# Kernel optimization log

Measured on AMD Instinct MI355X. Metric: run time of the kernel, lower is better.

The kernel has to match this reference:

```python
import jax, jax.numpy as jnp
import numpy as np

DIM = 256
NUM_HEADS = 4
HEAD_DIM = DIM // NUM_HEADS
SCALE = HEAD_DIM ** -0.5


def setup_inputs() -> dict:
    key = jax.random.key(0)
    ks = jax.random.split(key, 6)
    B, S = 4, 4096
    x = jax.random.normal(ks[0], (B, S, DIM), dtype=jnp.float32)
    # nn.Linear weights are [out, in]; we store them that way and apply x @ W.T
    wq = jax.random.normal(ks[1], (DIM, DIM), dtype=jnp.float32) * (DIM ** -0.5)
    wk = jax.random.normal(ks[2], (DIM, DIM), dtype=jnp.float32) * (DIM ** -0.5)
    wv = jax.random.normal(ks[3], (DIM, DIM), dtype=jnp.float32) * (DIM ** -0.5)
    wo = jax.random.normal(ks[4], (DIM, DIM), dtype=jnp.float32) * (DIM ** -0.5)
    bo = jax.random.normal(ks[5], (DIM,), dtype=jnp.float32) * 0.02
    return {"x": x, "wq": wq, "wk": wk, "wv": wv, "wo": wo, "bo": bo}


def reference(x, wq, wk, wv, wo, bo):
    B, S, D = x.shape
    H, Hd = NUM_HEADS, HEAD_DIM
    # project and split heads: [B, H, S, Hd]
    q = (x @ wq.T).reshape(B, S, H, Hd).transpose(0, 2, 1, 3)
    k = (x @ wk.T).reshape(B, S, H, Hd).transpose(0, 2, 1, 3)
    v = (x @ wv.T).reshape(B, S, H, Hd).transpose(0, 2, 1, 3)
    attn = jnp.einsum('bhqd,bhkd->bhqk', q, k) * SCALE
    attn = jax.nn.softmax(attn, axis=-1)  # dropout is identity in eval mode
    out = jnp.einsum('bhqk,bhkd->bhqd', attn, v)
    out = out.transpose(0, 2, 1, 3).reshape(B, S, D)
    return out @ wo.T + bo
```

## Files before the change

### kernel.cpp

```cpp
#include <hip/hip_runtime.h>
#include <hip/hip_bf16.h>
#include <stdint.h>

#define DIM    256
#define NH     4
#define HD     64
#define BATCH  4
#define SEQ    4096
#define NTOK   (BATCH*SEQ)

typedef __bf16    bf16_t;
typedef _Float16  f16_t;
typedef _Float16  f16x8  __attribute__((ext_vector_type(8)));
typedef _Float16  f16x4  __attribute__((ext_vector_type(4)));
typedef float     f32x4  __attribute__((ext_vector_type(4)));
typedef unsigned short u16x8 __attribute__((ext_vector_type(8)));

#define MFMA_F16    __builtin_amdgcn_mfma_f32_16x16x32_f16
#define MFMA_F16_16 __builtin_amdgcn_mfma_f32_16x16x16f16

#define QSCALE 0.18033688011112042f

#define WS_XA    ((size_t)0)
#define WS_Q     ((size_t)4194304)
#define WS_K     ((size_t)8388608)
#define WS_VT    ((size_t)12582912)
#define WS_W     ((size_t)16777216)
#define WS_BO    ((size_t)17039360)
#define WS_OATT  WS_XA

#define LSTRIDE 72
#define KBUF    4608

__device__ __forceinline__ size_t tiled_idx(int row, int k) {
  return ((size_t)(row >> 4) * 32 + (k >> 3)) * 128 + (row & 15) * 8 + (k & 7);
}

__device__ __forceinline__ int detect_mode(const uint32_t* wq_u32) {
  uint32_t word = wq_u32[(threadIdx.x & 63) * 431 + 17];
  uint32_t b = (word >> 8) & 0x7fu;
  unsigned long long m = __ballot(b >= 0x38u && b <= 0x3fu);
  return (__popcll(m) >= 32) ? 0 : 1;
}

__device__ __forceinline__ f16x8 cvt_chunk(const void* src, size_t elem, int mode) {
  f16x8 r;
  if (mode) {
    const float* s = (const float*)src + elem;
    #pragma unroll
    for (int j = 0; j < 8; ++j) r[j] = (f16_t)s[j];
  } else {
    u16x8 v = *(const u16x8*)((const unsigned short*)src + elem);
    #pragma unroll
    for (int j = 0; j < 8; ++j) r[j] = (f16_t)__uint_as_float(((unsigned)v[j]) << 16);
  }
  return r;
}

__global__ __launch_bounds__(256) void cvt_all_kernel(
    const void* __restrict__ x,
    const void* __restrict__ wq, const void* __restrict__ wk,
    const void* __restrict__ wv, const void* __restrict__ wo,
    const void* __restrict__ bo,
    f16_t* __restrict__ xA, f16_t* __restrict__ wT,
    float* __restrict__ bof) {
  __shared__ int s_mode;
  if (threadIdx.x < 64) {
    int m = detect_mode((const uint32_t*)wq);
    if (threadIdx.x == 0) s_mode = m;
  }
  __syncthreads();
  const int mode = s_mode;
  const int bid = blockIdx.x;

  if (bid < 2048) {
    int idx = bid * 256 + (int)threadIdx.x;
    int tok = idx >> 5, kc = idx & 31;
    f16x8 r = cvt_chunk(x, (size_t)tok * DIM + kc * 8, mode);
    *(f16x8*)(xA + tiled_idx(tok, kc * 8)) = r;
  } else if (bid < 2176) {
    int idx = (bid - 2048) * 256 + (int)threadIdx.x;
    int which = idx >> 13, local = idx & 8191;
    const void* src = (which == 0) ? wq : (which == 1) ? wk : (which == 2) ? wv : wo;
    int n = local >> 5, kc = local & 31;
    f16x8 r = cvt_chunk(src, (size_t)n * DIM + kc * 8, mode);
    *(f16x8*)(wT + (size_t)which * 65536 + tiled_idx(n, kc * 8)) = r;
  } else {
    int i = threadIdx.x;
    bof[i] = mode ? ((const float*)bo)[i] : (float)((const bf16_t*)bo)[i];
  }
}

__global__ __launch_bounds__(256) void proj_fused_kernel(
    const f16_t* __restrict__ xA, const f16_t* __restrict__ wT,
    f16_t* __restrict__ q, f16_t* __restrict__ kk, f16_t* __restrict__ vt) {
  const int z    = blockIdx.z;
  const f16_t* w = wT + (size_t)z * 65536;
  const int lane = threadIdx.x & 63;
  const int wvi  = threadIdx.x >> 6;
  const int c    = lane & 15;
  const int g    = lane >> 4;

  if (z < 2) {
    const float scale = (z == 0) ? QSCALE : 1.0f;
    f16_t* out = (z == 0) ? q : kk;
    const int m0 = blockIdx.x * 64 + wvi * 16;
    const int n0 = blockIdx.y * 64;
    const f16_t* abase = xA + (size_t)(m0 >> 4) * 4096 + c * 8;
    const f16_t* bbase = w + (size_t)(n0 >> 4) * 4096 + c * 8;
    f32x4 acc[4] = {};
    #pragma unroll
    for (int ks = 0; ks < 8; ++ks) {
      const int kc = (ks * 4 + g) * 128;
      f16x8 a = *(const f16x8*)(abase + kc);
      #pragma unroll
      for (int nt = 0; nt < 4; ++nt) {
        f16x8 b = *(const f16x8*)(bbase + (size_t)nt * 4096 + kc);
        acc[nt] = MFMA_F16(a, b, acc[nt], 0, 0, 0);
      }
    }
    #pragma unroll
    for (int nt = 0; nt < 4; ++nt) {
      const int n = n0 + nt * 16 + c;
      const int h = n >> 6, d = n & 63;
      #pragma unroll
      for (int r = 0; r < 4; ++r) {
        const int tok = m0 + g * 4 + r;
        const int b = tok >> 12, s = tok & 4095;
        out[(size_t)((b * NH + h) * SEQ + s) * HD + d] = (f16_t)(acc[nt][r] * scale);
      }
    }
  } else {
    const int m0 = blockIdx.y * 64 + wvi * 16;
    const int n0 = blockIdx.x * 64;
    const f16_t* abase = w + (size_t)(m0 >> 4) * 4096 + c * 8;
    const f16_t* bbase = xA + (size_t)(n0 >> 4) * 4096 + c * 8;
    f32x4 acc[4] = {};
    #pragma unroll
    for (int ks = 0; ks < 8; ++ks) {
      const int kc = (ks * 4 + g) * 128;
      f16x8 a = *(const f16x8*)(abase + kc);
      #pragma unroll
      for (int nt = 0; nt < 4; ++nt) {
        f16x8 b = *(const f16x8*)(bbase + (size_t)nt * 4096 + kc);
        acc[nt] = MFMA_F16(a, b, acc[nt], 0, 0, 0);
      }
    }
    #pragma unroll
    for (int nt = 0; nt < 4; ++nt) {
      const int tok = n0 + nt * 16 + c;
      const int b = tok >> 12, s = tok & 4095;
      #pragma unroll
      for (int r = 0; r < 4; ++r) {
        const int vd = m0 + g * 4 + r;
        const int h = vd >> 6, d = vd & 63;
        vt[(size_t)((b * NH + h) * HD + d) * SEQ + s] = (f16_t)acc[nt][r];
      }
    }
  }
}

__global__ __launch_bounds__(256, 4) void attn_kernel(
    const f16_t* __restrict__ q, const f16_t* __restrict__ k,
    const f16_t* __restrict__ vt, f16_t* __restrict__ o) {
  __shared__ __align__(16) f16_t smem[18432];

  const int tid  = threadIdx.x;
  const int lane = tid & 63;
  const int w    = tid >> 6;
  const int wq_  = w & 1;
  const int wk_  = w >> 1;
  const int c    = lane & 15;
  const int g    = lane >> 4;
  const int bh   = blockIdx.x;
  const int q0   = blockIdx.y * 64;

  const f16_t* qb = q + (size_t)(bh * SEQ + q0 + wq_ * 32 + c) * HD;
  f16x8 qf[2][2];
  #pragma unroll
  for (int qt = 0; qt < 2; ++qt) {
    qf[qt][0] = *(const f16x8*)(qb + (size_t)(qt * 16) * HD + g * 8);
    qf[qt][1] = *(const f16x8*)(qb + (size_t)(qt * 16) * HD + 32 + g * 8);
  }

  const int r0 = tid >> 3, ch = tid & 7;
  const f16_t* kg0 = k  + (size_t)bh * SEQ * HD + (size_t)r0 * HD + ch * 8;
  const f16_t* kg1 = kg0 + (size_t)32 * HD;
  const f16_t* vg0 = vt + (size_t)bh * HD * SEQ + (size_t)r0 * SEQ + ch * 8;
  const f16_t* vg1 = vg0 + (size_t)32 * SEQ;
  const int kst  = r0 * LSTRIDE + ch * 8;
  const int kst2 = (r0 + 32) * LSTRIDE + ch * 8;

  f32x4 oacc[8] = {};
  float lpart[2] = {};

  {
    uint4 ka  = *(const uint4*)(kg0);
    uint4 kb2 = *(const uint4*)(kg1);
    uint4 va  = *(const uint4*)(vg0);
    uint4 vb2 = *(const uint4*)(vg1);
    *(uint4*)(smem + kst)         = ka;
    *(uint4*)(smem + kst2)        = kb2;
    *(uint4*)(smem + KBUF + kst)  = va;
    *(uint4*)(smem + KBUF + kst2) = vb2;
  }
  __syncthreads();

  const int kAbase = (wk_ * 32 + c) * LSTRIDE + g * 8;
  const int vAbase = wk_ * 32 + g * 4;

  for (int kt = 0; kt < SEQ / 64; ++kt) {
    const int cur = (kt & 1) * (2 * KBUF);
    const int nxt = ((kt & 1) ^ 1) * (2 * KBUF);
    uint4 ka4, kb4, va4, vb4;
    const bool more = (kt < SEQ / 64 - 1);
    if (more) {
      const size_t ko = (size_t)(kt + 1) * 64 * HD;
      const size_t vo = (size_t)(kt + 1) * 64;
      ka4 = *(const uint4*)(kg0 + ko);
      kb4 = *(const uint4*)(kg1 + ko);
      va4 = *(const uint4*)(vg0 + vo);
      vb4 = *(const uint4*)(vg1 + vo);
    }

    f16x8 kfa[2][2];
    #pragma unroll
    for (int kts = 0; kts < 2; ++kts) {
      const f16_t* kl = smem + cur + kAbase + kts * 16 * LSTRIDE;
      kfa[kts][0] = *(const f16x8*)(kl);
      kfa[kts][1] = *(const f16x8*)(kl + 32);
    }
    f16x4 vfr[4][2];
    #pragma unroll
    for (int dt = 0; dt < 4; ++dt)
      #pragma unroll
      for (int kts = 0; kts < 2; ++kts)
        vfr[dt][kts] = *(const f16x4*)(smem + cur + KBUF +
                                       (dt * 16 + c) * LSTRIDE + vAbase + kts * 16);

    f16x4 pk[2][2];
    #pragma unroll
    for (int kts = 0; kts < 2; ++kts) {
      #pragma unroll
      for (int qt = 0; qt < 2; ++qt) {
        f32x4 st = {};
        st = MFMA_F16(kfa[kts][0], qf[qt][0], st, 0, 0, 0);
        st = MFMA_F16(kfa[kts][1], qf[qt][1], st, 0, 0, 0);
        float p0 = __builtin_amdgcn_exp2f(st[0]);
        float p1 = __builtin_amdgcn_exp2f(st[1]);
        float p2 = __builtin_amdgcn_exp2f(st[2]);
        float p3 = __builtin_amdgcn_exp2f(st[3]);
        lpart[qt] += (p0 + p1) + (p2 + p3);
        f16x4 pv = { (f16_t)p0, (f16_t)p1, (f16_t)p2, (f16_t)p3 };
        pk[kts][qt] = pv;
      }
    }
    #pragma unroll
    for (int dt = 0; dt < 4; ++dt)
      #pragma unroll
      for (int qt = 0; qt < 2; ++qt) {
        f32x4 acc = oacc[dt * 2 + qt];
        acc = MFMA_F16_16(vfr[dt][0], pk[0][qt], acc, 0, 0, 0);
        acc = MFMA_F16_16(vfr[dt][1], pk[1][qt], acc, 0, 0, 0);
        oacc[dt * 2 + qt] = acc;
      }

    if (more) {
      *(uint4*)(smem + nxt + kst)         = ka4;
      *(uint4*)(smem + nxt + kst2)        = kb4;
      *(uint4*)(smem + nxt + KBUF + kst)  = va4;
      *(uint4*)(smem + nxt + KBUF + kst2) = vb4;
    }
    __syncthreads();
  }

  float* red   = (float*)smem;
  float* lred_ = (float*)(smem + 16384);

  float lw[2];
  #pragma unroll
  for (int qt = 0; qt < 2; ++qt) {
    float lv = lpart[qt];
    lv += __shfl_xor(lv, 16);
    lv += __shfl_xor(lv, 32);
    lw[qt] = lv;
  }
  if (lane < 16) {
    #pragma unroll
    for (int qt = 0; qt < 2; ++qt) lred_[w * 32 + qt * 16 + lane] = lw[qt];
  }
  if (wk_ == 1) {
    float* dst = red + wq_ * 2048;
    #pragma unroll
    for (int i = 0; i < 8; ++i) *(f32x4*)(dst + i * 256 + lane * 4) = oacc[i];
  }
  __syncthreads();
  if (wk_ == 0) {
    const float* s = red + wq_ * 2048;
    #pragma unroll
    for (int i = 0; i < 8; ++i) oacc[i] += *(const f32x4*)(s + i * 256 + lane * 4);
    float inv[2];
    #pragma unroll
    for (int qt = 0; qt < 2; ++qt)
      inv[qt] = 1.0f / (lred_[w * 32 + qt * 16 + c] + lred_[(w + 2) * 32 + qt * 16 + c]);

    const int b = bh >> 2, h = bh & 3;
    #pragma unroll
    for (int dt = 0; dt < 4; ++dt) {
      #pragma unroll
      for (int qt = 0; qt < 2; ++qt) {
        f32x4 v = oacc[dt * 2 + qt];
        f16x4 ov = { (f16_t)(v[0] * inv[qt]), (f16_t)(v[1] * inv[qt]),
                     (f16_t)(v[2] * inv[qt]), (f16_t)(v[3] * inv[qt]) };
        const int mt = b * 256 + blockIdx.y * 4 + wq_ * 2 + qt;
        const int kc = h * 8 + dt * 2 + (g >> 1);
        *(f16x4*)(o + ((size_t)mt * 32 + kc) * 128 + c * 8 + (g & 1) * 4) = ov;
      }
    }
  }
}

__global__ __launch_bounds__(256) void out_proj_kernel(
    const f16_t* __restrict__ aA, const f16_t* __restrict__ wT,
    const float* __restrict__ bo, void* __restrict__ outv,
    const void* __restrict__ wq_raw) {
  __shared__ int s_mode;
  if (threadIdx.x < 64) {
    int m = detect_mode((const uint32_t*)wq_raw);
    if (threadIdx.x == 0) s_mode = m;
  }
  __syncthreads();
  const int mode = s_mode;

  const int lane = threadIdx.x & 63;
  const int wv   = threadIdx.x >> 6;
  const int c    = lane & 15;
  const int g    = lane >> 4;
  const int m0   = blockIdx.x * 64 + wv * 16;
  const int n0   = blockIdx.y * 64;

  const f16_t* abase = aA + (size_t)(m0 >> 4) * 4096 + c * 8;
  const f16_t* bbase = wT + (size_t)(n0 >> 4) * 4096 + c * 8;
  f32x4 acc[4] = {};

  #pragma unroll
  for (int ks = 0; ks < 8; ++ks) {
    const int kc = (ks * 4 + g) * 128;
    f16x8 a = *(const f16x8*)(abase + kc);
    #pragma unroll
    for (int nt = 0; nt < 4; ++nt) {
      f16x8 b = *(const f16x8*)(bbase + (size_t)nt * 4096 + kc);
      acc[nt] = MFMA_F16(a, b, acc[nt], 0, 0, 0);
    }
  }

  #pragma unroll
  for (int nt = 0; nt < 4; ++nt) {
    const int n = n0 + nt * 16 + c;
    const float bias = bo[n];
    #pragma unroll
    for (int r = 0; r < 4; ++r) {
      const int tok = m0 + g * 4 + r;
      const float val = acc[nt][r] + bias;
      const size_t idx = (size_t)tok * DIM + n;
      if (mode) ((float*)outv)[idx] = val;
      else      ((bf16_t*)outv)[idx] = (bf16_t)val;
    }
  }
}

extern "C" void kernel_launch(void* const* d_in, const int* in_sizes, int n_in,
                              void* d_out, int out_size, void* d_ws, size_t ws_size,
                              hipStream_t stream) {
  (void)in_sizes; (void)n_in; (void)out_size; (void)ws_size;
  const void* x  = d_in[0];
  const void* wq = d_in[1];
  const void* wk = d_in[2];
  const void* wv = d_in[3];
  const void* wo = d_in[4];
  const void* bo = d_in[5];

  f16_t* ws    = (f16_t*)d_ws;
  f16_t* xA    = ws + WS_XA;
  f16_t* q     = ws + WS_Q;
  f16_t* kk    = ws + WS_K;
  f16_t* vt    = ws + WS_VT;
  f16_t* wT    = ws + WS_W;
  f16_t* woT   = ws + WS_W + 196608;
  float* bof   = (float*)(ws + WS_BO);
  f16_t* oattA = ws + WS_OATT;

  cvt_all_kernel   <<<dim3(2177),      256, 0, stream>>>(x, wq, wk, wv, wo, bo,
                                                         xA, wT, bof);
  proj_fused_kernel<<<dim3(256, 4, 3), 256, 0, stream>>>(xA, wT, q, kk, vt);
  attn_kernel      <<<dim3(16, 64),    256, 0, stream>>>(q, kk, vt, oattA);
  out_proj_kernel  <<<dim3(256, 4),    256, 0, stream>>>(oattA, woT, bof, d_out, wq);
}
```

Baseline: 201.3 us.

## Rewrite attention with 32x32 MFMA, 128-query tiles and pre-swizzled K/V layouts

The attention kernel moves from 16x16 MFMA tiles to 32x32x16 MFMA, and each block now covers 128 queries instead of 64, halving the grid. The projection kernel writes K and V in a 64-row tile image with an XOR-swizzled chunk order, so the attention kernel can copy each tile to LDS contiguously and read it without bank conflicts. P fragments are rearranged in registers with permlane32 swaps. The aim is fewer MFMA issues, less LDS padding and cheaper loads, at the cost of more registers per thread (launch bounds drop to 2 blocks per CU) and a more intricate layout contract between kernels. Softmax still omits max subtraction, as before.

```diff
diff --git a/kernel.cpp b/kernel.cpp
--- a/kernel.cpp
+++ b/kernel.cpp
@@ -14,10 +14,14 @@
 typedef _Float16  f16x8  __attribute__((ext_vector_type(8)));
 typedef _Float16  f16x4  __attribute__((ext_vector_type(4)));
 typedef float     f32x4  __attribute__((ext_vector_type(4)));
+typedef float     f32x16 __attribute__((ext_vector_type(16)));
 typedef unsigned short u16x8 __attribute__((ext_vector_type(8)));
+typedef unsigned int   u32;
+typedef u32 u32x2 __attribute__((ext_vector_type(2)));
+typedef u32 u32x4 __attribute__((ext_vector_type(4)));
 
 #define MFMA_F16    __builtin_amdgcn_mfma_f32_16x16x32_f16
-#define MFMA_F16_16 __builtin_amdgcn_mfma_f32_16x16x16f16
+#define MFMA32_F16  __builtin_amdgcn_mfma_f32_32x32x16_f16
 
 #define QSCALE 0.18033688011112042f
 
@@ -29,9 +33,6 @@
 #define WS_BO    ((size_t)17039360)
 #define WS_OATT  WS_XA
 
-#define LSTRIDE 72
-#define KBUF    4608
-
 __device__ __forceinline__ size_t tiled_idx(int row, int k) {
   return ((size_t)(row >> 4) * 32 + (k >> 3)) * 128 + (row & 15) * 8 + (k & 7);
 }
@@ -55,6 +56,24 @@
     for (int j = 0; j < 8; ++j) r[j] = (f16_t)__uint_as_float(((unsigned)v[j]) << 16);
   }
   return r;
+}
+
+__device__ __forceinline__ u32 pkh(float a, float b) {
+  auto h = __builtin_amdgcn_cvt_pkrtz(a, b);
+  return __builtin_bit_cast(u32, h);
+}
+
+__device__ __forceinline__ void swap32(u32& x, u32& y) {
+#if __has_builtin(__builtin_amdgcn_permlane32_swap)
+  u32x2 r = __builtin_amdgcn_permlane32_swap(x, y, false, false);
+  x = r[0]; y = r[1];
+#else
+  u32 xp = __shfl_xor((int)x, 32), yp = __shfl_xor((int)y, 32);
+  const bool h = (threadIdx.x & 32) != 0;
+  u32 nx = h ? yp : x;
+  u32 ny = h ? y  : xp;
+  x = nx; y = ny;
+#endif
 }
 
 __global__ __launch_bounds__(256) void cvt_all_kernel(
@@ -103,7 +122,6 @@
 
   if (z < 2) {
     const float scale = (z == 0) ? QSCALE : 1.0f;
-    f16_t* out = (z == 0) ? q : kk;
     const int m0 = blockIdx.x * 64 + wvi * 16;
     const int n0 = blockIdx.y * 64;
     const f16_t* abase = xA + (size_t)(m0 >> 4) * 4096 + c * 8;
@@ -119,15 +137,32 @@
         acc[nt] = MFMA_F16(a, b, acc[nt], 0, 0, 0);
       }
     }
-    #pragma unroll
-    for (int nt = 0; nt < 4; ++nt) {
-      const int n = n0 + nt * 16 + c;
-      const int h = n >> 6, d = n & 63;
-      #pragma unroll
-      for (int r = 0; r < 4; ++r) {
-        const int tok = m0 + g * 4 + r;
-        const int b = tok >> 12, s = tok & 4095;
-        out[(size_t)((b * NH + h) * SEQ + s) * HD + d] = (f16_t)(acc[nt][r] * scale);
+    if (z == 0) {
+      #pragma unroll
+      for (int nt = 0; nt < 4; ++nt) {
+        const int n = n0 + nt * 16 + c;
+        const int h = n >> 6, d = n & 63;
+        #pragma unroll
+        for (int r = 0; r < 4; ++r) {
+          const int tok = m0 + g * 4 + r;
+          const int b = tok >> 12, s = tok & 4095;
+          q[(size_t)((b * NH + h) * SEQ + s) * HD + d] = (f16_t)(acc[nt][r] * scale);
+        }
+      }
+    } else {
+      #pragma unroll
+      for (int nt = 0; nt < 4; ++nt) {
+        const int n = n0 + nt * 16 + c;
+        const int h = n >> 6, d = n & 63;
+        #pragma unroll
+        for (int r = 0; r < 4; ++r) {
+          const int tok = m0 + g * 4 + r;
+          const int b = tok >> 12, s = tok & 4095;
+          const int kt = s >> 6, row = s & 63;
+          const int ch = (d >> 3) ^ (row & 7);
+          kk[(size_t)(b * NH + h) * (SEQ * HD) + kt * 4096 + row * 64 + ch * 8 + (d & 7)]
+              = (f16_t)acc[nt][r];
+        }
       }
     }
   } else {
@@ -150,173 +185,176 @@
     for (int nt = 0; nt < 4; ++nt) {
       const int tok = n0 + nt * 16 + c;
       const int b = tok >> 12, s = tok & 4095;
+      const int kt = s >> 6, ko = s & 63;
       #pragma unroll
       for (int r = 0; r < 4; ++r) {
         const int vd = m0 + g * 4 + r;
         const int h = vd >> 6, d = vd & 63;
-        vt[(size_t)((b * NH + h) * HD + d) * SEQ + s] = (f16_t)acc[nt][r];
-      }
-    }
-  }
-}
-
-__global__ __launch_bounds__(256, 4) void attn_kernel(
-    const f16_t* __restrict__ q, const f16_t* __restrict__ k,
-    const f16_t* __restrict__ vt, f16_t* __restrict__ o) {
-  __shared__ __align__(16) f16_t smem[18432];
-
-  const int tid  = threadIdx.x;
-  const int lane = tid & 63;
-  const int w    = tid >> 6;
-  const int wq_  = w & 1;
-  const int wk_  = w >> 1;
-  const int c    = lane & 15;
-  const int g    = lane >> 4;
-  const int bh   = blockIdx.x;
-  const int q0   = blockIdx.y * 64;
-
-  const f16_t* qb = q + (size_t)(bh * SEQ + q0 + wq_ * 32 + c) * HD;
-  f16x8 qf[2][2];
+        const int ch = (ko >> 3) ^ (d & 7);
+        vt[(size_t)(b * NH + h) * (SEQ * HD) + kt * 4096 + d * 64 + ch * 8 + (ko & 7)]
+            = (f16_t)acc[nt][r];
+      }
+    }
+  }
+}
+
+__global__ __launch_bounds__(256, 2) void attn_kernel(
+    const f16_t* __restrict__ q, const f16_t* __restrict__ kimg,
+    const f16_t* __restrict__ vimg, f16_t* __restrict__ o) {
+  __shared__ __align__(16) f16_t smem[16896];
+
+  const int tid = threadIdx.x;
+  const int l   = tid & 63;
+  const int w   = tid >> 6;
+  const int wq_ = w & 1;
+  const int wk_ = w >> 1;
+  const int ql  = l & 31;
+  const int hi  = l >> 5;
+  const int bh  = blockIdx.x;
+  const int q0  = blockIdx.y * 128;
+
+  const f16_t* qb = q + ((size_t)bh * SEQ + q0 + wq_ * 64 + ql) * HD + hi * 8;
+  f16x8 qf[2][4];
+  #pragma unroll
+  for (int qt = 0; qt < 2; ++qt)
+    #pragma unroll
+    for (int s = 0; s < 4; ++s)
+      qf[qt][s] = *(const f16x8*)(qb + (size_t)qt * 32 * HD + s * 16);
+
+  const bool isv = tid >= 128;
+  const f16_t* gsrc = (isv ? vimg : kimg) + (size_t)bh * (SEQ * HD) + (tid & 127) * 32;
+  f16_t* ldst = smem + (isv ? 4096 : 0) + (tid & 127) * 32;
+
+  const int qx  = ql & 7;
+  const int krow = wk_ * 32 + ql;
+  int koff[4], voff[2][2];
+  #pragma unroll
+  for (int s = 0; s < 4; ++s)
+    koff[s] = krow * 64 + (((s * 2 + hi) ^ qx) * 8);
+  #pragma unroll
+  for (int dt = 0; dt < 2; ++dt) {
+    const int drow = dt * 32 + ql;
+    #pragma unroll
+    for (int kb = 0; kb < 2; ++kb)
+      voff[dt][kb] = 4096 + drow * 64 + (((wk_ * 4 + kb * 2 + hi) ^ qx) * 8);
+  }
+
+  f32x16 acc[2][2] = {};
+  float lsum[2] = {0.f, 0.f};
+
+  {
+    const uint4* gg = (const uint4*)gsrc;
+    uint4* dd = (uint4*)ldst;
+    dd[0] = gg[0]; dd[1] = gg[1]; dd[2] = gg[2]; dd[3] = gg[3];
+  }
+  __syncthreads();
+
+  for (int kt = 0; kt < SEQ / 64; ++kt) {
+    const int bufo = (kt & 1) * 8192;
+    const bool more = kt < SEQ / 64 - 1;
+    uint4 s0, s1, s2, s3;
+    if (more) {
+      const uint4* gg = (const uint4*)(gsrc + (size_t)(kt + 1) * 4096);
+      s0 = gg[0]; s1 = gg[1]; s2 = gg[2]; s3 = gg[3];
+    }
+
+    f16x8 kf[4], vf[2][2];
+    #pragma unroll
+    for (int s = 0; s < 4; ++s)
+      kf[s] = *(const f16x8*)(smem + bufo + koff[s]);
+    #pragma unroll
+    for (int dt = 0; dt < 2; ++dt)
+      #pragma unroll
+      for (int kb = 0; kb < 2; ++kb)
+        vf[dt][kb] = *(const f16x8*)(smem + bufo + voff[dt][kb]);
+
+    f16x8 pf[2][2];
+    #pragma unroll
+    for (int qt = 0; qt < 2; ++qt) {
+      f32x16 st = {};
+      #pragma unroll
+      for (int s = 0; s < 4; ++s) st = MFMA32_F16(kf[s], qf[qt][s], st, 0, 0, 0);
+      float p[16];
+      #pragma unroll
+      for (int r = 0; r < 16; ++r) p[r] = __builtin_amdgcn_exp2f(st[r]);
+      float ls = 0.f;
+      #pragma unroll
+      for (int r = 0; r < 16; r += 4) ls += (p[r] + p[r + 1]) + (p[r + 2] + p[r + 3]);
+      lsum[qt] += ls;
+      #pragma unroll
+      for (int kb = 0; kb < 2; ++kb) {
+        u32 d0 = pkh(p[kb * 8 + 0], p[kb * 8 + 1]);
+        u32 d1 = pkh(p[kb * 8 + 2], p[kb * 8 + 3]);
+        u32 d2 = pkh(p[kb * 8 + 4], p[kb * 8 + 5]);
+        u32 d3 = pkh(p[kb * 8 + 6], p[kb * 8 + 7]);
+        swap32(d0, d2);
+        swap32(d1, d3);
+        u32x4 fd; fd[0] = d0; fd[1] = d1; fd[2] = d2; fd[3] = d3;
+        pf[qt][kb] = __builtin_bit_cast(f16x8, fd);
+      }
+    }
+
+    #pragma unroll
+    for (int dt = 0; dt < 2; ++dt)
+      #pragma unroll
+      for (int qt = 0; qt < 2; ++qt) {
+        f32x16 a = acc[dt][qt];
+        a = MFMA32_F16(vf[dt][0], pf[qt][0], a, 0, 0, 0);
+        a = MFMA32_F16(vf[dt][1], pf[qt][1], a, 0, 0, 0);
+        acc[dt][qt] = a;
+      }
+
+    if (more) {
+      uint4* dd = (uint4*)(ldst + (bufo ^ 8192));
+      dd[0] = s0; dd[1] = s1; dd[2] = s2; dd[3] = s3;
+    }
+    __syncthreads();
+  }
+
+  float* lred = (float*)(smem + 16384);
   #pragma unroll
   for (int qt = 0; qt < 2; ++qt) {
-    qf[qt][0] = *(const f16x8*)(qb + (size_t)(qt * 16) * HD + g * 8);
-    qf[qt][1] = *(const f16x8*)(qb + (size_t)(qt * 16) * HD + 32 + g * 8);
-  }
-
-  const int r0 = tid >> 3, ch = tid & 7;
-  const f16_t* kg0 = k  + (size_t)bh * SEQ * HD + (size_t)r0 * HD + ch * 8;
-  const f16_t* kg1 = kg0 + (size_t)32 * HD;
-  const f16_t* vg0 = vt + (size_t)bh * HD * SEQ + (size_t)r0 * SEQ + ch * 8;
-  const f16_t* vg1 = vg0 + (size_t)32 * SEQ;
-  const int kst  = r0 * LSTRIDE + ch * 8;
-  const int kst2 = (r0 + 32) * LSTRIDE + ch * 8;
-
-  f32x4 oacc[8] = {};
-  float lpart[2] = {};
-
-  {
-    uint4 ka  = *(const uint4*)(kg0);
-    uint4 kb2 = *(const uint4*)(kg1);
-    uint4 va  = *(const uint4*)(vg0);
-    uint4 vb2 = *(const uint4*)(vg1);
-    *(uint4*)(smem + kst)         = ka;
-    *(uint4*)(smem + kst2)        = kb2;
-    *(uint4*)(smem + KBUF + kst)  = va;
-    *(uint4*)(smem + KBUF + kst2) = vb2;
-  }
-  __syncthreads();
-
-  const int kAbase = (wk_ * 32 + c) * LSTRIDE + g * 8;
-  const int vAbase = wk_ * 32 + g * 4;
-
-  for (int kt = 0; kt < SEQ / 64; ++kt) {
-    const int cur = (kt & 1) * (2 * KBUF);
-    const int nxt = ((kt & 1) ^ 1) * (2 * KBUF);
-    uint4 ka4, kb4, va4, vb4;
-    const bool more = (kt < SEQ / 64 - 1);
-    if (more) {
-      const size_t ko = (size_t)(kt + 1) * 64 * HD;
-      const size_t vo = (size_t)(kt + 1) * 64;
-      ka4 = *(const uint4*)(kg0 + ko);
-      kb4 = *(const uint4*)(kg1 + ko);
-      va4 = *(const uint4*)(vg0 + vo);
-      vb4 = *(const uint4*)(vg1 + vo);
-    }
-
-    f16x8 kfa[2][2];
-    #pragma unroll
-    for (int kts = 0; kts < 2; ++kts) {
-      const f16_t* kl = smem + cur + kAbase + kts * 16 * LSTRIDE;
-      kfa[kts][0] = *(const f16x8*)(kl);
-      kfa[kts][1] = *(const f16x8*)(kl + 32);
-    }
-    f16x4 vfr[4][2];
-    #pragma unroll
-    for (int dt = 0; dt < 4; ++dt)
-      #pragma unroll
-      for (int kts = 0; kts < 2; ++kts)
-        vfr[dt][kts] = *(const f16x4*)(smem + cur + KBUF +
-                                       (dt * 16 + c) * LSTRIDE + vAbase + kts * 16);
-
-    f16x4 pk[2][2];
-    #pragma unroll
-    for (int kts = 0; kts < 2; ++kts) {
-      #pragma unroll
-      for (int qt = 0; qt < 2; ++qt) {
-        f32x4 st = {};
-        st = MFMA_F16(kfa[kts][0], qf[qt][0], st, 0, 0, 0);
-        st = MFMA_F16(kfa[kts][1], qf[qt][1], st, 0, 0, 0);
-        float p0 = __builtin_amdgcn_exp2f(st[0]);
-        float p1 = __builtin_amdgcn_exp2f(st[1]);
-        float p2 = __builtin_amdgcn_exp2f(st[2]);
-        float p3 = __builtin_amdgcn_exp2f(st[3]);
-        lpart[qt] += (p0 + p1) + (p2 + p3);
-        f16x4 pv = { (f16_t)p0, (f16_t)p1, (f16_t)p2, (f16_t)p3 };
-        pk[kts][qt] = pv;
-      }
-    }
-    #pragma unroll
-    for (int dt = 0; dt < 4; ++dt)
-      #pragma unroll
-      for (int qt = 0; qt < 2; ++qt) {
-        f32x4 acc = oacc[dt * 2 + qt];
-        acc = MFMA_F16_16(vfr[dt][0], pk[0][qt], acc, 0, 0, 0);
-        acc = MFMA_F16_16(vfr[dt][1], pk[1][qt], acc, 0, 0, 0);
-        oacc[dt * 2 + qt] = acc;
-      }
-
-    if (more) {
-      *(uint4*)(smem + nxt + kst)         = ka4;
-      *(uint4*)(smem + nxt + kst2)        = kb4;
-      *(uint4*)(smem + nxt + KBUF + kst)  = va4;
-      *(uint4*)(smem + nxt + KBUF + kst2) = vb4;
-    }
-    __syncthreads();
-  }
-
-  float* red   = (float*)smem;
-  float* lred_ = (float*)(smem + 16384);
-
-  float lw[2];
-  #pragma unroll
-  for (int qt = 0; qt < 2; ++qt) {
-    float lv = lpart[qt];
-    lv += __shfl_xor(lv, 16);
-    lv += __shfl_xor(lv, 32);
-    lw[qt] = lv;
-  }
-  if (lane < 16) {
-    #pragma unroll
-    for (int qt = 0; qt < 2; ++qt) lred_[w * 32 + qt * 16 + lane] = lw[qt];
-  }
+    lsum[qt] += __shfl_xor(lsum[qt], 32);
+    if (hi == 0) lred[w * 64 + qt * 32 + ql] = lsum[qt];
+  }
+  float* red = (float*)smem;
   if (wk_ == 1) {
-    float* dst = red + wq_ * 2048;
-    #pragma unroll
-    for (int i = 0; i < 8; ++i) *(f32x4*)(dst + i * 256 + lane * 4) = oacc[i];
+    #pragma unroll
+    for (int t = 0; t < 4; ++t) {
+      f32x16 a = acc[t >> 1][t & 1];
+      #pragma unroll
+      for (int qd = 0; qd < 4; ++qd) {
+        f32x4 v = { a[qd * 4], a[qd * 4 + 1], a[qd * 4 + 2], a[qd * 4 + 3] };
+        *(f32x4*)(red + wq_ * 4096 + (t * 4 + qd) * 256 + l * 4) = v;
+      }
+    }
   }
   __syncthreads();
   if (wk_ == 0) {
-    const float* s = red + wq_ * 2048;
-    #pragma unroll
-    for (int i = 0; i < 8; ++i) oacc[i] += *(const f32x4*)(s + i * 256 + lane * 4);
     float inv[2];
     #pragma unroll
     for (int qt = 0; qt < 2; ++qt)
-      inv[qt] = 1.0f / (lred_[w * 32 + qt * 16 + c] + lred_[(w + 2) * 32 + qt * 16 + c]);
+      inv[qt] = 1.0f / (lred[w * 64 + qt * 32 + ql] + lred[(w + 2) * 64 + qt * 32 + ql]);
 
     const int b = bh >> 2, h = bh & 3;
     #pragma unroll
-    for (int dt = 0; dt < 4; ++dt) {
+    for (int dt = 0; dt < 2; ++dt)
       #pragma unroll
       for (int qt = 0; qt < 2; ++qt) {
-        f32x4 v = oacc[dt * 2 + qt];
-        f16x4 ov = { (f16_t)(v[0] * inv[qt]), (f16_t)(v[1] * inv[qt]),
-                     (f16_t)(v[2] * inv[qt]), (f16_t)(v[3] * inv[qt]) };
-        const int mt = b * 256 + blockIdx.y * 4 + wq_ * 2 + qt;
-        const int kc = h * 8 + dt * 2 + (g >> 1);
-        *(f16x4*)(o + ((size_t)mt * 32 + kc) * 128 + c * 8 + (g & 1) * 4) = ov;
-      }
-    }
+        const int t = dt * 2 + qt;
+        f32x16 a = acc[dt][qt];
+        const int tokg = b * SEQ + q0 + wq_ * 64 + qt * 32 + ql;
+        const size_t rowbase = (size_t)(tokg >> 4) * 32 * 128 + (tokg & 15) * 8 + hi * 4;
+        #pragma unroll
+        for (int qd = 0; qd < 4; ++qd) {
+          f32x4 v = *(const f32x4*)(red + wq_ * 4096 + (t * 4 + qd) * 256 + l * 4);
+          f16x4 ov = { (f16_t)((a[qd * 4 + 0] + v[0]) * inv[qt]),
+                       (f16_t)((a[qd * 4 + 1] + v[1]) * inv[qt]),
+                       (f16_t)((a[qd * 4 + 2] + v[2]) * inv[qt]),
+                       (f16_t)((a[qd * 4 + 3] + v[3]) * inv[qt]) };
+          *(f16x4*)(o + rowbase + (size_t)(h * 8 + dt * 4 + qd) * 128) = ov;
+        }
+      }
   }
 }
 
@@ -393,6 +431,6 @@
   cvt_all_kernel   <<<dim3(2177),      256, 0, stream>>>(x, wq, wk, wv, wo, bo,
                                                          xA, wT, bof);
   proj_fused_kernel<<<dim3(256, 4, 3), 256, 0, stream>>>(xA, wT, q, kk, vt);
-  attn_kernel      <<<dim3(16, 64),    256, 0, stream>>>(q, kk, vt, oattA);
+  attn_kernel      <<<dim3(16, 32),    256, 0, stream>>>(q, kk, vt, oattA);
   out_proj_kernel  <<<dim3(256, 4),    256, 0, stream>>>(oattA, woT, bof, d_out, wq);
 }
```

Measured after the change: 191.0 us. 5.1% less time.
